# Kernel tuning notes

Measured on AMD Instinct MI355X. Metric: run time of the kernel, lower is better.

The kernel has to match this reference:

```python
import jax, jax.numpy as jnp
import numpy as np

N = 40000       # nodes
E = 400000      # directed edges (before self-loops)
F_IN = 50       # PPI num_features
HID = 64        # per-head hidden
H = 4           # heads
NCLS = 121      # PPI num_classes
NEG_SLOPE = 0.2


def gat_layer(x, src, dst, W, a_src, a_dst, W_res, b, concat):
    """PyG GATConv: per-edge attention, segment softmax over dst, scatter-add."""
    n = x.shape[0]
    h, c = a_src.shape
    feat = (x @ W).reshape(n, h, c)                       # [N,H,C]
    al_s = (feat * a_src[None]).sum(-1)                   # [N,H]
    al_d = (feat * a_dst[None]).sum(-1)                   # [N,H]
    e = jax.nn.leaky_relu(al_s[src] + al_d[dst], NEG_SLOPE)  # [E,H]
    m = jax.ops.segment_max(e, dst, num_segments=n)       # stable softmax max
    e = jnp.exp(e - m[dst])
    denom = jax.ops.segment_sum(e, dst, num_segments=n)
    w = e / (denom[dst] + 1e-16)                          # [E,H] attention
    msg = feat[src] * w[:, :, None]                       # [E,H,C]
    out = jax.ops.segment_sum(msg, dst, num_segments=n)   # [N,H,C]
    out = out.reshape(n, h * c) if concat else out.mean(axis=1)
    return out + x @ W_res + b                            # residual proj + bias


def setup_inputs() -> dict:
    key = jax.random.key(0)
    ks = jax.random.split(key, 18)
    g = lambda k, shape: jax.random.normal(k, shape, dtype=jnp.float32) * 0.1
    return {
        "x": jax.random.normal(ks[0], (N, F_IN), dtype=jnp.float32),
        "edge_index": jax.random.randint(ks[1], (2, E), 0, N, dtype=jnp.int32),
        "W1": g(ks[2], (F_IN, H * HID)), "a1s": g(ks[3], (H, HID)), "a1d": g(ks[4], (H, HID)),
        "Wr1": g(ks[5], (F_IN, H * HID)), "b1": jnp.zeros((H * HID,), jnp.float32),
        "W2": g(ks[6], (H * HID, H * HID)), "a2s": g(ks[7], (H, HID)), "a2d": g(ks[8], (H, HID)),
        "Wr2": g(ks[9], (H * HID, H * HID)), "b2": jnp.zeros((H * HID,), jnp.float32),
        "W3": g(ks[10], (H * HID, H * NCLS)), "a3s": g(ks[11], (H, NCLS)), "a3d": g(ks[12], (H, NCLS)),
        "Wr3": g(ks[13], (H * HID, NCLS)), "b3": jnp.zeros((NCLS,), jnp.float32),
    }


def reference(x, edge_index, W1, a1s, a1d, Wr1, b1, W2, a2s, a2d, Wr2, b2,
              W3, a3s, a3d, Wr3, b3):
    loop = jnp.arange(N, dtype=edge_index.dtype)          # add_self_loops=True
    src = jnp.concatenate([edge_index[0], loop])
    dst = jnp.concatenate([edge_index[1], loop])
    h = jax.nn.relu(gat_layer(x, src, dst, W1, a1s, a1d, Wr1, b1, True))
    h = jax.nn.relu(gat_layer(h, src, dst, W2, a2s, a2d, Wr2, b2, True))
    return gat_layer(h, src, dst, W3, a3s, a3d, Wr3, b3, False)
```

## Files before the change

### kernel.cpp

```cpp
#include <hip/hip_runtime.h>
#include <hip/hip_bf16.h>


#define NNODES 40000
#define MPAD   40064
#define NEDGES 400000
#define FIN    50
#define NHEAD  4
#define SCANB  157
#define N4     160000

typedef __attribute__((ext_vector_type(8))) short short8;
typedef __attribute__((ext_vector_type(4))) float float4v;
typedef __attribute__((ext_vector_type(4))) unsigned short ushort4v;
typedef __attribute__((ext_vector_type(8))) unsigned short ushort8v;

__device__ inline unsigned short f2bf(float f) {
    union { float f; unsigned u; } v; v.f = f;
    unsigned r = v.u + 0x7fff + ((v.u >> 16) & 1);
    return (unsigned short)(r >> 16);
}
__device__ inline float bf2f(unsigned short u) {
    union { unsigned u; float f; } v; v.u = ((unsigned)u) << 16; return v.f;
}
__device__ inline float lrelu(float x) { return x >= 0.f ? x : 0.2f * x; }

__global__ void hist_kernel(const int* __restrict__ dst, int* __restrict__ counts, int E) {
    int i = blockIdx.x * blockDim.x + threadIdx.x;
    if (i < E) atomicAdd(&counts[dst[i]], 1);
}

__global__ __launch_bounds__(256) void scan_local(const int* __restrict__ counts,
                                                  int* __restrict__ offsets,
                                                  int* __restrict__ partials) {
    __shared__ int sh[256];
    int b = blockIdx.x, t = threadIdx.x, i = b * 256 + t;
    int v = (i < NNODES) ? counts[i] : 0;
    sh[t] = v;
    __syncthreads();
    #pragma unroll
    for (int off = 1; off < 256; off <<= 1) {
        int u = (t >= off) ? sh[t - off] : 0;
        __syncthreads();
        sh[t] += u;
        __syncthreads();
    }
    if (i < NNODES) offsets[i] = sh[t] - v;
    if (t == 255) partials[b] = sh[255];
}

__global__ __launch_bounds__(256) void scan_partials(int* __restrict__ partials,
                                                     int* __restrict__ pexcl) {
    __shared__ int sh[256];
    int t = threadIdx.x;
    int v = (t < SCANB) ? partials[t] : 0;
    sh[t] = v;
    __syncthreads();
    #pragma unroll
    for (int off = 1; off < 256; off <<= 1) {
        int u = (t >= off) ? sh[t - off] : 0;
        __syncthreads();
        sh[t] += u;
        __syncthreads();
    }
    pexcl[t] = sh[t] - v;
}

__global__ __launch_bounds__(256) void scan_carry(int* __restrict__ offsets,
                                                  const int* __restrict__ pexcl) {
    int b = blockIdx.x, i = b * 256 + threadIdx.x;
    if (i < NNODES) offsets[i] += pexcl[b];
}

__global__ void scatter_kernel(const int* __restrict__ src, const int* __restrict__ dst,
                               int* __restrict__ offsets,
                               int* __restrict__ csr_src, int* __restrict__ csr_dst, int E) {
    int i = blockIdx.x * blockDim.x + threadIdx.x;
    if (i < E) {
        int d = dst[i];
        int pos = atomicAdd(&offsets[d], 1);
        csr_src[pos] = src[i];
        csr_dst[pos] = d;
    }
}

__global__ void edge_p(const float* __restrict__ al4,
                       const int* __restrict__ csr_src, const int* __restrict__ csr_dst,
                       float* __restrict__ p4, int E) {
    int j = blockIdx.x * blockDim.x + threadIdx.x;
    if (j >= E) return;
    int s = csr_src[j], d = csr_dst[j];
    float4v a0 = *(const float4v*)&al4[s * 4];
    float4v a1 = *(const float4v*)&al4[2 * N4 + s * 4];
    float4v b0 = *(const float4v*)&al4[N4 + d * 4];
    float4v b1 = *(const float4v*)&al4[3 * N4 + d * 4];
    float4v p;
    p.x = __expf(lrelu(a0.x + a1.x + b0.x + b1.x));
    p.y = __expf(lrelu(a0.y + a1.y + b0.y + b1.y));
    p.z = __expf(lrelu(a0.z + a1.z + b0.z + b1.z));
    p.w = __expf(lrelu(a0.w + a1.w + b0.w + b1.w));
    *(float4v*)&p4[(size_t)j * 4] = p;
}

__global__ void convert_x(const float* __restrict__ x, short* __restrict__ xb) {
    int i = blockIdx.x * blockDim.x + threadIdx.x;
    if (i >= MPAD * 64) return;
    int r = i >> 6, k = i & 63;
    float v = (r < NNODES && k < FIN) ? x[r * FIN + k] : 0.f;
    xb[i] = f2bf(v);
}

__global__ void convert_pack1(const float* __restrict__ W1, const float* __restrict__ Wr1,
                              const float* __restrict__ W2, const float* __restrict__ Wr2,
                              short* __restrict__ wc1, short* __restrict__ wc2) {
    int i = blockIdx.x * blockDim.x + threadIdx.x;
    if (i < 32768) {
        const float* W = (i < 16384) ? W1 : Wr1;
        int j = i & 16383;
        int n = j >> 6, k = j & 63;
        wc1[i] = f2bf((k < FIN) ? W[k * 256 + n] : 0.f);
    } else if (i < 163840) {
        int j = (i - 32768) & 65535;
        const float* W = (i < 98304) ? W2 : Wr2;
        int n = j >> 8, k = j & 255;
        wc2[(i - 32768)] = f2bf(W[k * 256 + n]);
    }
}

__global__ void convert_pack2(const float* __restrict__ W3, const float* __restrict__ Wr3,
                              const float* __restrict__ a3s, const float* __restrict__ a3d,
                              short* __restrict__ wc3,
                              float* __restrict__ a3sp, float* __restrict__ a3dp) {
    int i = blockIdx.x * blockDim.x + threadIdx.x;
    if (i < 131072) {
        int j = i >> 8, k = i & 255;
        int h = j >> 7, c = j & 127;
        wc3[i] = f2bf((c < 121) ? W3[k * 484 + h * 121 + c] : 0.f);
    } else if (i < 163840) {
        int j = i - 131072;
        int n = j >> 8, k = j & 255;
        wc3[131072 + j] = f2bf((n < 121) ? Wr3[k * 121 + n] : 0.f);
    } else if (i < 164864) {
        int j = i - 163840;
        int which = j >> 9; int jj = j & 511;
        int h = jj >> 7, c = jj & 127;
        float v = (c < 121) ? (which ? a3d[h * 121 + c] : a3s[h * 121 + c]) : 0.f;
        (which ? a3dp : a3sp)[jj] = v;
    }
}

template<int MODE>
__global__ __launch_bounds__(256) void mfma_gemm_fused(const short* __restrict__ A,
                                                       const short* __restrict__ Bt,
                                                       const float* __restrict__ bias,
                                                       const float* __restrict__ asv,
                                                       const float* __restrict__ adv,
                                                       unsigned short* __restrict__ Fb,
                                                       unsigned short* __restrict__ Rb,
                                                       float* __restrict__ out,
                                                       float* __restrict__ al4,
                                                       int Kp) {
    const int NW = MODE ? 512 : 256;
    __shared__ __align__(16) short As[4096];
    __shared__ __align__(16) unsigned short Cs[2][32][132];
    const int tid = threadIdx.x;
    const int l   = tid & 63;
    const int w   = tid >> 6;
    const int wm  = w >> 1, wn = w & 1;
    const int row0 = blockIdx.y * 128;
    const int col0 = blockIdx.x * 128;
    const int lrow = l & 15;
    const int lq   = l >> 4;
    const int sr = (tid >> 6) * 16 + (tid & 15);
    const int sk = ((tid >> 4) & 3) * 8;

    float4v acc[4][4] = {};

    for (int k0 = 0; k0 < Kp; k0 += 32) {
        short8 a0 = *(const short8*)&A[(size_t)(row0 + sr) * Kp + k0 + sk];
        short8 a1 = *(const short8*)&A[(size_t)(row0 + 64 + sr) * Kp + k0 + sk];
        short8 bfrag[4];
        #pragma unroll
        for (int ct = 0; ct < 4; ++ct) {
            int col = col0 + wn * 64 + ct * 16 + lrow;
            bfrag[ct] = *(const short8*)&Bt[(size_t)col * Kp + k0 + lq * 8];
        }
        __syncthreads();
        *(short8*)&As[tid * 8] = a0;
        *(short8*)&As[(tid + 256) * 8] = a1;
        __syncthreads();
        #pragma unroll
        for (int rt = 0; rt < 4; ++rt) {
            short8 afrag = *(const short8*)&As[(wm * 4 + rt) * 512 + l * 8];
            #pragma unroll
            for (int ct = 0; ct < 4; ++ct)
                acc[rt][ct] = __builtin_amdgcn_mfma_f32_16x16x32_bf16(afrag, bfrag[ct],
                                                                      acc[rt][ct], 0, 0, 0);
        }
    }

    const int colbase = col0 + wn * 64;
    const bool isW = colbase < NW;

    if (isW) {
        const int head = (colbase * NHEAD) / NW;
        const int half = MODE ? ((colbase >> 6) & 1) : 0;
        float* als_o = al4 + (half ? 2 * N4 : 0);
        float* ald_o = als_o + N4;
        float as_c[4], ad_c[4];
        #pragma unroll
        for (int ct = 0; ct < 4; ++ct) {
            int col = colbase + ct * 16 + lrow;
            as_c[ct] = asv[col];
            ad_c[ct] = adv[col];
        }
        #pragma unroll
        for (int rt = 0; rt < 4; ++rt) {
            #pragma unroll
            for (int i = 0; i < 4; ++i) {
                int r = row0 + wm * 64 + rt * 16 + lq * 4 + i;
                float fs = 0.f, fd = 0.f;
                #pragma unroll
                for (int ct = 0; ct < 4; ++ct) {
                    float v = acc[rt][ct][i];
                    fs += v * as_c[ct];
                    fd += v * ad_c[ct];
                }
                #pragma unroll
                for (int o2 = 8; o2; o2 >>= 1) {
                    fs += __shfl_xor(fs, o2, 16);
                    fd += __shfl_xor(fd, o2, 16);
                }
                if (lrow == 0 && r < NNODES) {
                    als_o[r * 4 + head] = fs;
                    ald_o[r * 4 + head] = fd;
                }
            }
        }
    }

    if (MODE == 1 && col0 >= 512) {
        #pragma unroll
        for (int ct = 0; ct < 4; ++ct) {
            int c = colbase + ct * 16 + lrow - 512;
            if (c >= 121) continue;
            float bv = bias[c];
            #pragma unroll
            for (int rt = 0; rt < 4; ++rt) {
                int rbase = row0 + wm * 64 + rt * 16 + lq * 4;
                #pragma unroll
                for (int i = 0; i < 4; ++i) {
                    int r = rbase + i;
                    if (r < NNODES) out[(size_t)r * 121 + c] = acc[rt][ct][i] + bv;
                }
            }
        }
        return;
    }

    const bool isRb = (MODE == 0) && (col0 >= 256);
    unsigned short* dest = isRb ? Rb : Fb;
    const int ldd = MODE ? 512 : 256;
    const int cold = isRb ? col0 - 256 : col0;
    float badd[4] = {0.f, 0.f, 0.f, 0.f};
    if (isRb) {
        #pragma unroll
        for (int ct = 0; ct < 4; ++ct)
            badd[ct] = bias[col0 - 256 + wn * 64 + ct * 16 + lrow];
    }

    const int rp = tid >> 2, g = rp >> 5, rr = rp & 31, q = tid & 3;
    #pragma unroll
    for (int p = 0; p < 2; ++p) {
        if (p) __syncthreads();
        #pragma unroll
        for (int rt2 = 0; rt2 < 2; ++rt2) {
            int rt = p * 2 + rt2;
            #pragma unroll
            for (int ct = 0; ct < 4; ++ct) {
                int cl = wn * 64 + ct * 16 + lrow;
                #pragma unroll
                for (int i = 0; i < 4; ++i) {
                    int lr = rt2 * 16 + lq * 4 + i;
                    Cs[wm][lr][cl] = f2bf(acc[rt][ct][i] + badd[ct]);
                }
            }
        }
        __syncthreads();
        int grow = row0 + g * 64 + p * 32 + rr;
        if (grow < NNODES) {
            #pragma unroll
            for (int k = 0; k < 4; ++k) {
                ushort8v v = *(const ushort8v*)&Cs[g][rr][q * 32 + 8 * k];
                *(ushort8v*)&dest[(size_t)grow * ldd + cold + q * 32 + 8 * k] = v;
            }
        }
    }
}

__global__ __launch_bounds__(256) void attn64_kernel(const unsigned short* __restrict__ featb,
                                                     const float* __restrict__ al4,
                                                     const int* __restrict__ offs,
                                                     const int* __restrict__ csr,
                                                     const float* __restrict__ p4,
                                                     const unsigned short* __restrict__ Rb,
                                                     unsigned short* __restrict__ outb) {
    int n = blockIdx.x * 4 + (threadIdx.x >> 6);
    int l = threadIdx.x & 63;
    int h = l >> 4;
    int beg = n ? offs[n - 1] : 0;
    int end = offs[n];

    float lg = al4[n * 4 + h] + al4[2 * N4 + n * 4 + h]
             + al4[N4 + n * 4 + h] + al4[3 * N4 + n * 4 + h];
    float p0 = __expf(lrelu(lg));
    float s = p0;
    float a0, a1, a2, a3;
    {
        ushort4v f = *(const ushort4v*)&featb[(size_t)n * 256 + 4 * l];
        a0 = p0 * bf2f(f.x); a1 = p0 * bf2f(f.y); a2 = p0 * bf2f(f.z); a3 = p0 * bf2f(f.w);
    }
    #pragma unroll 8
    for (int j = beg; j < end; ++j) {
        int sn = csr[j];
        float p = p4[(size_t)j * 4 + h];
        s += p;
        ushort4v f = *(const ushort4v*)&featb[(size_t)sn * 256 + 4 * l];
        a0 += p * bf2f(f.x); a1 += p * bf2f(f.y); a2 += p * bf2f(f.z); a3 += p * bf2f(f.w);
    }
    float inv = 1.f / s;
    ushort4v r = *(const ushort4v*)&Rb[(size_t)n * 256 + 4 * l];
    ushort4v o;
    o.x = f2bf(fmaxf(bf2f(r.x) + a0 * inv, 0.f));
    o.y = f2bf(fmaxf(bf2f(r.y) + a1 * inv, 0.f));
    o.z = f2bf(fmaxf(bf2f(r.z) + a2 * inv, 0.f));
    o.w = f2bf(fmaxf(bf2f(r.w) + a3 * inv, 0.f));
    *(ushort4v*)&outb[(size_t)n * 256 + 4 * l] = o;
}

__global__ __launch_bounds__(256) void attn121_kernel(const unsigned short* __restrict__ featb,
                                                      const float* __restrict__ al4,
                                                      const int* __restrict__ offs,
                                                      const int* __restrict__ csr,
                                                      const float* __restrict__ p4,
                                                      float* __restrict__ out) {
    int n = blockIdx.x * 4 + (threadIdx.x >> 6);
    int l = threadIdx.x & 63;
    int h = l >> 4;
    int beg = n ? offs[n - 1] : 0;
    int end = offs[n];

    float lg = al4[n * 4 + h] + al4[2 * N4 + n * 4 + h]
             + al4[N4 + n * 4 + h] + al4[3 * N4 + n * 4 + h];
    float p0 = __expf(lrelu(lg));
    float s = p0;
    float a[8];
    {
        ushort8v f = *(const ushort8v*)&featb[(size_t)n * 512 + 8 * l];
        #pragma unroll
        for (int i = 0; i < 8; ++i) a[i] = p0 * bf2f(f[i]);
    }
    #pragma unroll 4
    for (int j = beg; j < end; ++j) {
        int sn = csr[j];
        float p = p4[(size_t)j * 4 + h];
        s += p;
        ushort8v f = *(const ushort8v*)&featb[(size_t)sn * 512 + 8 * l];
        #pragma unroll
        for (int i = 0; i < 8; ++i) a[i] += p * bf2f(f[i]);
    }
    float inv = 0.25f / s;
    #pragma unroll
    for (int i = 0; i < 8; ++i) {
        a[i] *= inv;
        a[i] += __shfl_xor(a[i], 16, 64);
        a[i] += __shfl_xor(a[i], 32, 64);
    }
    if (l < 16) {
        #pragma unroll
        for (int i = 0; i < 8; ++i) {
            int c = 8 * l + i;
            if (c < 121) out[(size_t)n * 121 + c] += a[i];
        }
    }
}

extern "C" void kernel_launch(void* const* d_in, const int* in_sizes, int n_in,
                              void* d_out, int out_size, void* d_ws, size_t ws_size,
                              hipStream_t stream) {
    const float* x   = (const float*)d_in[0];
    const int* ei    = (const int*)d_in[1];
    const float* W1  = (const float*)d_in[2];
    const float* a1s = (const float*)d_in[3];
    const float* a1d = (const float*)d_in[4];
    const float* Wr1 = (const float*)d_in[5];
    const float* b1  = (const float*)d_in[6];
    const float* W2  = (const float*)d_in[7];
    const float* a2s = (const float*)d_in[8];
    const float* a2d = (const float*)d_in[9];
    const float* Wr2 = (const float*)d_in[10];
    const float* b2  = (const float*)d_in[11];
    const float* W3  = (const float*)d_in[12];
    const float* a3s = (const float*)d_in[13];
    const float* a3d = (const float*)d_in[14];
    const float* Wr3 = (const float*)d_in[15];
    const float* b3  = (const float*)d_in[16];
    float* out = (float*)d_out;

    const int* e_src = ei;
    const int* e_dst = ei + NEDGES;

    char* ws = (char*)d_ws;
    size_t off = 0;
    auto carve = [&](size_t bytes) { void* p = ws + off; off += (bytes + 255) & ~255ull; return p; };
    unsigned short* Fb = (unsigned short*)carve((size_t)MPAD * 512 * 2);
    unsigned short* Rb = (unsigned short*)carve((size_t)MPAD * 256 * 2);
    unsigned short* Hb = (unsigned short*)carve((size_t)MPAD * 256 * 2);
    short* xb   = (short*)carve((size_t)MPAD * 64 * 2);
    short* wc1  = (short*)carve((size_t)512 * 64 * 2);
    short* wc2  = (short*)carve((size_t)512 * 256 * 2);
    short* wc3  = (short*)carve((size_t)640 * 256 * 2);
    float* a3sp = (float*)carve(512 * 4);
    float* a3dp = (float*)carve(512 * 4);
    float* al4  = (float*)carve((size_t)4 * N4 * 4);
    float* p4   = (float*)carve((size_t)NEDGES * 4 * 4);
    int* csr_src = (int*)carve((size_t)NEDGES * 4);
    int* csr_dst = (int*)carve((size_t)NEDGES * 4);
    int* offsets = (int*)carve(((size_t)NNODES + 4) * 4);
    int* counts  = (int*)carve((size_t)NNODES * 4);
    int* partials = (int*)carve(256 * 4);
    int* pexcl    = (int*)carve(256 * 4);

    const int EB = (NEDGES + 255) / 256;
    dim3 blk(256);

    convert_x<<<(MPAD * 64 + 255) / 256, blk, 0, stream>>>(x, xb);
    convert_pack1<<<(163840 + 255) / 256, blk, 0, stream>>>(W1, Wr1, W2, Wr2, wc1, wc2);
    convert_pack2<<<(164864 + 255) / 256, blk, 0, stream>>>(W3, Wr3, a3s, a3d, wc3, a3sp, a3dp);

    hipMemsetAsync(al4 + 2 * N4, 0, (size_t)2 * N4 * 4, stream);

    hipMemsetAsync(counts, 0, NNODES * 4, stream);
    hist_kernel<<<EB, blk, 0, stream>>>(e_dst, counts, NEDGES);
    scan_local<<<SCANB, blk, 0, stream>>>(counts, offsets, partials);
    scan_partials<<<1, blk, 0, stream>>>(partials, pexcl);
    scan_carry<<<SCANB, blk, 0, stream>>>(offsets, pexcl);
    scatter_kernel<<<EB, blk, 0, stream>>>(e_src, e_dst, offsets, csr_src, csr_dst, NEDGES);

    mfma_gemm_fused<0><<<dim3(4, 313), blk, 0, stream>>>(xb, wc1, b1, a1s, a1d,
                                                         Fb, Rb, nullptr, al4, 64);
    edge_p<<<EB, blk, 0, stream>>>(al4, csr_src, csr_dst, p4, NEDGES);
    attn64_kernel<<<NNODES / 4, blk, 0, stream>>>(Fb, al4, offsets, csr_src, p4, Rb, Hb);

    mfma_gemm_fused<0><<<dim3(4, 313), blk, 0, stream>>>((short*)Hb, wc2, b2, a2s, a2d,
                                                         Fb, Rb, nullptr, al4, 256);
    edge_p<<<EB, blk, 0, stream>>>(al4, csr_src, csr_dst, p4, NEDGES);
    attn64_kernel<<<NNODES / 4, blk, 0, stream>>>(Fb, al4, offsets, csr_src, p4, Rb, Hb);

    mfma_gemm_fused<1><<<dim3(5, 313), blk, 0, stream>>>((short*)Hb, wc3, b3, a3sp, a3dp,
                                                         Fb, nullptr, out, al4, 256);
    edge_p<<<EB, blk, 0, stream>>>(al4, csr_src, csr_dst, p4, NEDGES);
    attn121_kernel<<<NNODES / 4, blk, 0, stream>>>(Fb, al4, offsets, csr_src, p4, out);
}
```

Baseline: 469.1 us.

## Use fp8 features for layer-3 gather and split edges across half-waves

Adds a kernel that converts the layer-3 bf16 feature matrix to packed fp8, and the final attention kernel now gathers fp8 rows, halving the bytes read per edge. Both attention kernels now split each node's edge list between the two half-waves, with each lane handling more features, and combine the partial sums with lane shuffles. The goal is to cut random-gather memory traffic and expose more loads in flight. The cost is an extra conversion pass and write of the fp8 buffer, plus reduced precision in the last layer's aggregation.

```diff
diff --git a/kernel.cpp b/kernel.cpp
--- a/kernel.cpp
+++ b/kernel.cpp
@@ -12,8 +12,10 @@
 
 typedef __attribute__((ext_vector_type(8))) short short8;
 typedef __attribute__((ext_vector_type(4))) float float4v;
+typedef __attribute__((ext_vector_type(2))) float float2v;
 typedef __attribute__((ext_vector_type(4))) unsigned short ushort4v;
 typedef __attribute__((ext_vector_type(8))) unsigned short ushort8v;
+typedef __attribute__((ext_vector_type(4))) unsigned int uint4v;
 
 __device__ inline unsigned short f2bf(float f) {
     union { float f; unsigned u; } v; v.f = f;
@@ -147,6 +149,16 @@
         float v = (c < 121) ? (which ? a3d[h * 121 + c] : a3s[h * 121 + c]) : 0.f;
         (which ? a3dp : a3sp)[jj] = v;
     }
+}
+
+__global__ void convert_f8(const unsigned short* __restrict__ Fb, unsigned int* __restrict__ F8) {
+    int i = blockIdx.x * blockDim.x + threadIdx.x;
+    if (i >= NNODES * 128) return;
+    ushort4v f = *(const ushort4v*)&Fb[(size_t)i * 4];
+    int v = 0;
+    v = __builtin_amdgcn_cvt_pk_fp8_f32(bf2f(f.x), bf2f(f.y), v, false);
+    v = __builtin_amdgcn_cvt_pk_fp8_f32(bf2f(f.z), bf2f(f.w), v, true);
+    F8[i] = (unsigned int)v;
 }
 
 template<int MODE>
@@ -307,38 +319,46 @@
                                                      unsigned short* __restrict__ outb) {
     int n = blockIdx.x * 4 + (threadIdx.x >> 6);
     int l = threadIdx.x & 63;
-    int h = l >> 4;
+    int half = l >> 5, li = l & 31;
+    int h = li >> 3;
     int beg = n ? offs[n - 1] : 0;
     int end = offs[n];
+
+    float a[8] = {};
+    float s = 0.f;
+    #pragma unroll 4
+    for (int j = beg + half; j < end; j += 2) {
+        int sn = csr[j];
+        float p = p4[(size_t)j * 4 + h];
+        s += p;
+        ushort8v f = *(const ushort8v*)&featb[(size_t)sn * 256 + 8 * li];
+        #pragma unroll
+        for (int i = 0; i < 8; ++i) a[i] += p * bf2f(f[i]);
+    }
+    s += __shfl_xor(s, 32, 64);
+    #pragma unroll
+    for (int i = 0; i < 8; ++i) a[i] += __shfl_xor(a[i], 32, 64);
 
     float lg = al4[n * 4 + h] + al4[2 * N4 + n * 4 + h]
              + al4[N4 + n * 4 + h] + al4[3 * N4 + n * 4 + h];
     float p0 = __expf(lrelu(lg));
-    float s = p0;
-    float a0, a1, a2, a3;
+    s += p0;
     {
-        ushort4v f = *(const ushort4v*)&featb[(size_t)n * 256 + 4 * l];
-        a0 = p0 * bf2f(f.x); a1 = p0 * bf2f(f.y); a2 = p0 * bf2f(f.z); a3 = p0 * bf2f(f.w);
-    }
-    #pragma unroll 8
-    for (int j = beg; j < end; ++j) {
-        int sn = csr[j];
-        float p = p4[(size_t)j * 4 + h];
-        s += p;
-        ushort4v f = *(const ushort4v*)&featb[(size_t)sn * 256 + 4 * l];
-        a0 += p * bf2f(f.x); a1 += p * bf2f(f.y); a2 += p * bf2f(f.z); a3 += p * bf2f(f.w);
-    }
-    float inv = 1.f / s;
-    ushort4v r = *(const ushort4v*)&Rb[(size_t)n * 256 + 4 * l];
-    ushort4v o;
-    o.x = f2bf(fmaxf(bf2f(r.x) + a0 * inv, 0.f));
-    o.y = f2bf(fmaxf(bf2f(r.y) + a1 * inv, 0.f));
-    o.z = f2bf(fmaxf(bf2f(r.z) + a2 * inv, 0.f));
-    o.w = f2bf(fmaxf(bf2f(r.w) + a3 * inv, 0.f));
-    *(ushort4v*)&outb[(size_t)n * 256 + 4 * l] = o;
-}
-
-__global__ __launch_bounds__(256) void attn121_kernel(const unsigned short* __restrict__ featb,
+        ushort8v f = *(const ushort8v*)&featb[(size_t)n * 256 + 8 * li];
+        #pragma unroll
+        for (int i = 0; i < 8; ++i) a[i] += p0 * bf2f(f[i]);
+    }
+    if (half == 0) {
+        float inv = 1.f / s;
+        ushort8v r = *(const ushort8v*)&Rb[(size_t)n * 256 + 8 * li];
+        ushort8v o;
+        #pragma unroll
+        for (int i = 0; i < 8; ++i) o[i] = f2bf(fmaxf(bf2f(r[i]) + a[i] * inv, 0.f));
+        *(ushort8v*)&outb[(size_t)n * 256 + 8 * li] = o;
+    }
+}
+
+__global__ __launch_bounds__(256) void attn121_kernel(const unsigned int* __restrict__ F8,
                                                       const float* __restrict__ al4,
                                                       const int* __restrict__ offs,
                                                       const int* __restrict__ csr,
@@ -346,40 +366,56 @@
                                                       float* __restrict__ out) {
     int n = blockIdx.x * 4 + (threadIdx.x >> 6);
     int l = threadIdx.x & 63;
-    int h = l >> 4;
+    int half = l >> 5, li = l & 31;
+    int h = li >> 3;
     int beg = n ? offs[n - 1] : 0;
     int end = offs[n];
+
+    float a[16] = {};
+    float s = 0.f;
+    #pragma unroll 2
+    for (int j = beg + half; j < end; j += 2) {
+        int sn = csr[j];
+        float p = p4[(size_t)j * 4 + h];
+        s += p;
+        uint4v u = *(const uint4v*)&F8[(size_t)sn * 128 + 4 * li];
+        #pragma unroll
+        for (int k = 0; k < 4; ++k) {
+            float2v lo = __builtin_amdgcn_cvt_pk_f32_fp8(u[k], false);
+            float2v hi = __builtin_amdgcn_cvt_pk_f32_fp8(u[k], true);
+            a[4 * k + 0] += p * lo.x; a[4 * k + 1] += p * lo.y;
+            a[4 * k + 2] += p * hi.x; a[4 * k + 3] += p * hi.y;
+        }
+    }
+    s += __shfl_xor(s, 32, 64);
+    #pragma unroll
+    for (int i = 0; i < 16; ++i) a[i] += __shfl_xor(a[i], 32, 64);
 
     float lg = al4[n * 4 + h] + al4[2 * N4 + n * 4 + h]
              + al4[N4 + n * 4 + h] + al4[3 * N4 + n * 4 + h];
     float p0 = __expf(lrelu(lg));
-    float s = p0;
-    float a[8];
+    s += p0;
     {
-        ushort8v f = *(const ushort8v*)&featb[(size_t)n * 512 + 8 * l];
-        #pragma unroll
-        for (int i = 0; i < 8; ++i) a[i] = p0 * bf2f(f[i]);
-    }
-    #pragma unroll 4
-    for (int j = beg; j < end; ++j) {
-        int sn = csr[j];
-        float p = p4[(size_t)j * 4 + h];
-        s += p;
-        ushort8v f = *(const ushort8v*)&featb[(size_t)sn * 512 + 8 * l];
-        #pragma unroll
-        for (int i = 0; i < 8; ++i) a[i] += p * bf2f(f[i]);
+        uint4v u = *(const uint4v*)&F8[(size_t)n * 128 + 4 * li];
+        #pragma unroll
+        for (int k = 0; k < 4; ++k) {
+            float2v lo = __builtin_amdgcn_cvt_pk_f32_fp8(u[k], false);
+            float2v hi = __builtin_amdgcn_cvt_pk_f32_fp8(u[k], true);
+            a[4 * k + 0] += p0 * lo.x; a[4 * k + 1] += p0 * lo.y;
+            a[4 * k + 2] += p0 * hi.x; a[4 * k + 3] += p0 * hi.y;
+        }
     }
     float inv = 0.25f / s;
     #pragma unroll
-    for (int i = 0; i < 8; ++i) {
+    for (int i = 0; i < 16; ++i) {
         a[i] *= inv;
+        a[i] += __shfl_xor(a[i], 8, 64);
         a[i] += __shfl_xor(a[i], 16, 64);
-        a[i] += __shfl_xor(a[i], 32, 64);
-    }
-    if (l < 16) {
-        #pragma unroll
-        for (int i = 0; i < 8; ++i) {
-            int c = 8 * l + i;
+    }
+    if (l < 8) {
+        #pragma unroll
+        for (int i = 0; i < 16; ++i) {
+            int c = 16 * l + i;
             if (c < 121) out[(size_t)n * 121 + c] += a[i];
         }
     }
@@ -416,6 +452,7 @@
     unsigned short* Fb = (unsigned short*)carve((size_t)MPAD * 512 * 2);
     unsigned short* Rb = (unsigned short*)carve((size_t)MPAD * 256 * 2);
     unsigned short* Hb = (unsigned short*)carve((size_t)MPAD * 256 * 2);
+    unsigned int* F8 = (unsigned int*)carve((size_t)NNODES * 128 * 4);
     short* xb   = (short*)carve((size_t)MPAD * 64 * 2);
     short* wc1  = (short*)carve((size_t)512 * 64 * 2);
     short* wc2  = (short*)carve((size_t)512 * 256 * 2);
@@ -459,6 +496,7 @@
 
     mfma_gemm_fused<1><<<dim3(5, 313), blk, 0, stream>>>((short*)Hb, wc3, b3, a3sp, a3dp,
                                                          Fb, nullptr, out, al4, 256);
+    convert_f8<<<(NNODES * 128 + 255) / 256, blk, 0, stream>>>(Fb, F8);
     edge_p<<<EB, blk, 0, stream>>>(al4, csr_src, csr_dst, p4, NEDGES);
-    attn121_kernel<<<NNODES / 4, blk, 0, stream>>>(Fb, al4, offsets, csr_src, p4, out);
-}
+    attn121_kernel<<<NNODES / 4, blk, 0, stream>>>(F8, al4, offsets, csr_src, p4, out);
+}
```

Result: faster. 452.5 us (-3.5%).
